# Kernel tuning notes

Measured on AMD Instinct MI355X. Metric: run time of the kernel, lower is better.

Reference implementation:

```python
import jax, jax.numpy as jnp
import numpy as np

THRESHOLD = 0.99


def setup_inputs() -> dict:
    key = jax.random.key(0)
    k1, k2, k3 = jax.random.split(key, 3)
    B, T, D, L = 8, 2048, 1024, 4
    x = jax.random.normal(k1, (B, T, D), dtype=jnp.float32)
    # per-step sub-layer weights (Linear(D, D)), scaled like typical init
    layer_w = jax.random.normal(k2, (L, D, D), dtype=jnp.float32) * (1.0 / np.sqrt(D))
    layer_b = jnp.zeros((L, D), dtype=jnp.float32)
    halt_w = jax.random.normal(k3, (D, 1), dtype=jnp.float32) * (1.0 / np.sqrt(D))
    halt_b = jnp.zeros((1,), dtype=jnp.float32)
    return {"x": x, "layer_w": layer_w, "layer_b": layer_b,
            "halt_w": halt_w, "halt_b": halt_b}


def reference(x, layer_w, layer_b, halt_w, halt_b):
    # Adaptive Computation Time forward.
    # x: (B,T,D); layer_w: (L,D,D); halt_w: (D,1)
    n_steps = layer_w.shape[0]
    B, T, D = x.shape
    dtype = x.dtype
    output = jnp.zeros((B, T, D), dtype=dtype)
    cumulative_halt = jnp.zeros((B, T, 1), dtype=dtype)
    remainder = jnp.ones((B, T, 1), dtype=dtype)
    ponder_steps = jnp.zeros((B, T, 1), dtype=dtype)
    h = x
    for step_idx in range(n_steps):  # small fixed layer count
        # sub-layer: Linear + GELU, (B,T,D) -> (B,T,D)
        h = jax.nn.gelu(jnp.einsum('btd,de->bte', h, layer_w[step_idx]) + layer_b[step_idx])
        # halting unit: Linear(D,1) + sigmoid -> (B,T,1)
        p = jax.nn.sigmoid(h @ halt_w + halt_b)
        if step_idx == n_steps - 1:
            weight = remainder
            contrib = remainder  # all tokens forced to halt
        else:
            halt_mask = (cumulative_halt + p) >= THRESHOLD
            weight = jnp.where(halt_mask, remainder, p)
            contrib = weight
        output = output + weight * h
        ponder_steps = ponder_steps + weight
        cumulative_halt = cumulative_halt + contrib
        remainder = jnp.clip(1.0 - cumulative_halt, 0.0)
    ponder_cost = ponder_steps.mean()
    return output, ponder_cost
```

## Files before the change

### kernel.cpp

```cpp
#include <hip/hip_runtime.h>

typedef __attribute__((ext_vector_type(8))) short short8;
typedef __attribute__((ext_vector_type(4))) float f32x4;
typedef __attribute__((ext_vector_type(4))) unsigned short u16x4;
typedef unsigned short u16;

#define D_DIM 1024
#define NKT 32

__device__ __forceinline__ u16 f2bf(float f) {
  unsigned u = __builtin_bit_cast(unsigned, f);
  u += 0x7fffu + ((u >> 16) & 1u);
  return (u16)(u >> 16);
}
__device__ __forceinline__ float bf2f(u16 b) {
  return __builtin_bit_cast(float, ((unsigned)b) << 16);
}
__device__ __forceinline__ float gelu_f(float x) {
  float i = 0.7978845608028654f * (x + 0.044715f * x * x * x);
  float ex = __builtin_amdgcn_exp2f(i * 2.885390081777927f);
  float th = 1.0f - 2.0f * __builtin_amdgcn_rcpf(ex + 1.0f);
  return 0.5f * x * (1.0f + th);
}
__device__ __forceinline__ f32x4 mfma16(short8 a, short8 b, f32x4 c) {
  return __builtin_amdgcn_mfma_f32_16x16x32_bf16(a, b, c, 0, 0, 0);
}
__device__ __forceinline__ void glds16(const u16* g, const u16* l) {
  __builtin_amdgcn_global_load_lds(
      (const __attribute__((address_space(1))) void*)g,
      (__attribute__((address_space(3))) void*)l, 16, 0, 0);
}

__global__ __launch_bounds__(256) void prep_kernel(
    const float* __restrict__ W, u16* __restrict__ Wth,
    const float* __restrict__ x, u16* __restrict__ xh, int* __restrict__ counts,
    int M) {
  __shared__ float tile[64][65];
  const int bid = blockIdx.x;
  const int t = threadIdx.x;
  if (bid < 1024) {
    const int k0 = (bid & 15) * 64, n0 = ((bid >> 4) & 15) * 64;
    const size_t lbase = (size_t)(bid >> 8) * D_DIM * D_DIM;
#pragma unroll
    for (int j = 0; j < 16; ++j) {
      int idx = t + 256 * j;
      int r = idx >> 6, c = idx & 63;
      tile[r][c] = W[lbase + (size_t)(k0 + r) * D_DIM + (n0 + c)];
    }
    __syncthreads();
#pragma unroll
    for (int j = 0; j < 16; ++j) {
      int idx = t + 256 * j;
      int r = idx >> 6, c = idx & 63;
      Wth[lbase + (size_t)(n0 + r) * D_DIM + (k0 + c)] = f2bf(tile[c][r]);
    }
  } else {
    if (bid == 1024 && t == 0) {
      counts[0] = M;
      counts[1] = M;
    }
    size_t i = ((size_t)(bid - 1024) * 256 + t) * 4;
    const float4 v = *(const float4*)(x + i);
    const float fv[4] = {v.x, v.y, v.z, v.w};
    u16x4 h4;
#pragma unroll
    for (int c = 0; c < 4; ++c) h4[c] = f2bf(fv[c]);
    *(u16x4*)(xh + i) = h4;
  }
}

__global__ __launch_bounds__(256, 4) void gemm_act_kernel(
    const u16* __restrict__ Ahp, const u16* __restrict__ Bhp,
    const float* __restrict__ bias, const float* __restrict__ halt_w,
    u16* __restrict__ Hh, float* __restrict__ zpart,
    const int* __restrict__ srcmap, const int* __restrict__ npadp, int M) {
  extern __shared__ u16 lds[];
  const int bid = blockIdx.x;
  const int mt = (bid & 7) + 8 * (bid >> 6);
  const int bm0 = mt * 128;
  if (bm0 >= *npadp) return;
  const int bn0 = ((bid >> 3) & 7) * 128;
  const int t = threadIdx.x;
  const int lane = t & 63, wid = t >> 6;
  const int wr = wid >> 1, wc = wid & 1;
  const int g = lane >> 4, r16 = lane & 15;

  const int lrow = lane >> 2;
  const int lchunk = (lane & 3) ^ ((lane >> 3) & 3);
  const int u0 = 2 * wid;
  int ar0 = bm0 + 16 * u0 + lrow, ar1 = ar0 + 16;
  if (srcmap) {
    ar0 = srcmap[ar0];
    ar1 = srcmap[ar1];
  }
  const int br0 = bn0 + 16 * u0 + lrow, br1 = br0 + 16;
  const u16* aSh0 = Ahp + (size_t)ar0 * D_DIM + lchunk * 8;
  const u16* aSh1 = Ahp + (size_t)ar1 * D_DIM + lchunk * 8;
  const u16* bSh0 = Bhp + (size_t)br0 * D_DIM + lchunk * 8;
  const u16* bSh1 = Bhp + (size_t)br1 * D_DIM + lchunk * 8;
  const int dst0 = u0 * 512 + lane * 8, dst1 = dst0 + 512;

  const int fsw = ((g ^ (r16 >> 1)) & 3) * 8;
  int a_rd[4], b_rd[4];
#pragma unroll
  for (int i = 0; i < 4; ++i) {
    a_rd[i] = (wr * 64 + i * 16 + r16) * 32 + fsw;
    b_rd[i] = 4096 + (wc * 64 + i * 16 + r16) * 32 + fsw;
  }

  f32x4 acc[4][4];
#pragma unroll
  for (int i = 0; i < 4; ++i)
#pragma unroll
    for (int j = 0; j < 4; ++j) acc[i][j] = (f32x4)0.0f;

  auto stage = [&](int kt) {
    const int k0 = kt << 5;
    u16* db = lds + (kt & 1) * 8192;
    glds16(aSh0 + k0, db + dst0);
    glds16(aSh1 + k0, db + dst1);
    glds16(bSh0 + k0, db + 4096 + dst0);
    glds16(bSh1 + k0, db + 4096 + dst1);
  };
  stage(0);

#pragma unroll 1
  for (int kt = 0; kt < NKT; ++kt) {
    asm volatile("s_waitcnt vmcnt(0)" ::: "memory");
    __builtin_amdgcn_s_barrier();
    asm volatile("" ::: "memory");
    const u16* Lb = lds + (kt & 1) * 8192;
    if (kt + 1 < NKT) stage(kt + 1);
    short8 ah[4], bh[4];
#pragma unroll
    for (int i = 0; i < 4; ++i) {
      ah[i] = *(const short8*)(Lb + a_rd[i]);
      bh[i] = *(const short8*)(Lb + b_rd[i]);
    }
    __builtin_amdgcn_s_setprio(1);
#pragma unroll
    for (int i = 0; i < 4; ++i)
#pragma unroll
      for (int n = 0; n < 4; ++n) acc[i][n] = mfma16(ah[i], bh[n], acc[i][n]);
    __builtin_amdgcn_s_setprio(0);
  }

  __syncthreads();

  float bv[4], hwv[4];
#pragma unroll
  for (int ni = 0; ni < 4; ++ni) {
    int col = bn0 + wc * 64 + ni * 16 + r16;
    bv[ni] = bias[col];
    hwv[ni] = halt_w[col];
  }
  float zp[4][4];
#pragma unroll
  for (int mi = 0; mi < 4; ++mi)
#pragma unroll
    for (int j = 0; j < 4; ++j) {
      float zz = 0.0f;
#pragma unroll
      for (int ni = 0; ni < 4; ++ni) {
        float v = gelu_f(acc[mi][ni][j] + bv[ni]);
        acc[mi][ni][j] = v;
        zz += v * hwv[ni];
      }
      zp[mi][j] = zz;
    }
#pragma unroll
  for (int off = 1; off < 16; off <<= 1)
#pragma unroll
    for (int mi = 0; mi < 4; ++mi)
#pragma unroll
      for (int j = 0; j < 4; ++j) zp[mi][j] += __shfl_xor(zp[mi][j], off);
  float* zf = (float*)lds;
  if (r16 == 0) {
#pragma unroll
    for (int mi = 0; mi < 4; ++mi)
#pragma unroll
      for (int j = 0; j < 4; ++j)
        zf[wc * 128 + wr * 64 + mi * 16 + g * 4 + j] = zp[mi][j];
  }
  __syncthreads();
  if (t < 128) zpart[(size_t)(bn0 >> 7) * M + bm0 + t] = zf[t] + zf[128 + t];
  __syncthreads();

  u16* hp = lds;
#pragma unroll
  for (int mi = 0; mi < 4; ++mi)
#pragma unroll
    for (int ni = 0; ni < 4; ++ni)
#pragma unroll
      for (int j = 0; j < 4; ++j)
        hp[(wr * 64 + mi * 16 + g * 4 + j) * 128 + wc * 64 + ni * 16 + r16] =
            f2bf(acc[mi][ni][j]);
  __syncthreads();
#pragma unroll
  for (int p = 0; p < 8; ++p) {
    int idx = p * 256 + t;
    int r = idx >> 4, c = idx & 15;
    *(short8*)(Hh + (size_t)(bm0 + r) * D_DIM + bn0 + c * 8) =
        *(const short8*)&hp[r * 128 + c * 8];
  }
}

__global__ __launch_bounds__(256) void act_weights_kernel(
    const float* __restrict__ zpart, const float* __restrict__ halt_b,
    float* __restrict__ cum, float* __restrict__ rem, float* __restrict__ pond,
    float* __restrict__ wout, float* __restrict__ wfull,
    int* __restrict__ slotmap, int* __restrict__ last_step,
    const int* __restrict__ idx, const int* __restrict__ np, int step,
    int last, int M) {
  int slot = blockIdx.x * 256 + threadIdx.x;
  if (slot >= *np) return;
  int tok = idx ? idx[slot] : slot;
  float z = halt_b[0];
#pragma unroll
  for (int nb = 0; nb < 8; ++nb) z += zpart[(size_t)nb * M + slot];
  float p = 1.0f / (1.0f + expf(-z));
  float c, r, q;
  if (step == 0) {
    c = 0.0f; r = 1.0f; q = 0.0f;
  } else {
    c = cum[tok]; r = rem[tok]; q = pond[tok];
  }
  float weight = last ? r : (((c + p) >= 0.99f) ? r : p);
  q += weight;
  c += weight;
  r = fmaxf(1.0f - c, 0.0f);
  cum[tok] = c;
  rem[tok] = r;
  pond[tok] = q;
  wout[slot] = weight;
  wfull[(size_t)step * M + tok] = weight;
  slotmap[(size_t)step * M + tok] = slot;
  last_step[tok] = step;
}

__global__ __launch_bounds__(1024) void compact_kernel(
    const float* __restrict__ rem, const int* __restrict__ idx_cur,
    const int* __restrict__ ncur_p, int* __restrict__ idx_next,
    int* __restrict__ src_next, int* __restrict__ cnt_next) {
  __shared__ int sc[1024];
  const int t = threadIdx.x;
  const int n = *ncur_p;
  const int base = t * 16;
  int lc = 0;
#pragma unroll
  for (int i = 0; i < 16; ++i) {
    int j = base + i;
    if (j < n) {
      int tok = idx_cur ? idx_cur[j] : j;
      if (rem[tok] > 0.0f) ++lc;
    }
  }
  sc[t] = lc;
  __syncthreads();
  for (int d = 1; d < 1024; d <<= 1) {
    int v = (t >= d) ? sc[t - d] : 0;
    __syncthreads();
    sc[t] += v;
    __syncthreads();
  }
  int pos = sc[t] - lc;
  const int total = sc[1023];
#pragma unroll
  for (int i = 0; i < 16; ++i) {
    int j = base + i;
    if (j < n) {
      int tok = idx_cur ? idx_cur[j] : j;
      if (rem[tok] > 0.0f) {
        idx_next[pos] = tok;
        src_next[pos] = j;
        ++pos;
      }
    }
  }
  if (t == 0) {
    int pad = (total + 127) & ~127;
    cnt_next[0] = total;
    cnt_next[1] = pad;
    for (int j = total; j < pad; ++j) {
      idx_next[j] = -1;
      src_next[j] = 0;
    }
  }
}

__global__ __launch_bounds__(256) void act_out_kernel(
    const u16* __restrict__ h, const float* __restrict__ w,
    const int* __restrict__ idx, const int* __restrict__ np, int accum,
    float* __restrict__ out) {
  size_t gid = (size_t)blockIdx.x * 256 + threadIdx.x;
  int slot = (int)(gid >> 7);
  if (slot >= *np) return;
  int off = ((int)gid & 127) * 8;
  int tok = idx ? idx[slot] : slot;
  size_t hb = (size_t)slot * D_DIM + off;
  size_t ob = (size_t)tok * D_DIM + off;
  float ws = w[slot];
  short8 hi = *(const short8*)(h + hb);
  float o[8];
  if (accum) {
    float4 a = *(const float4*)(out + ob);
    float4 b = *(const float4*)(out + ob + 4);
    o[0] = a.x; o[1] = a.y; o[2] = a.z; o[3] = a.w;
    o[4] = b.x; o[5] = b.y; o[6] = b.z; o[7] = b.w;
  } else {
#pragma unroll
    for (int j = 0; j < 8; ++j) o[j] = 0.0f;
  }
#pragma unroll
  for (int j = 0; j < 8; ++j) o[j] += ws * bf2f((u16)hi[j]);
  *(float4*)(out + ob) = make_float4(o[0], o[1], o[2], o[3]);
  *(float4*)(out + ob + 4) = make_float4(o[4], o[5], o[6], o[7]);
}

__global__ __launch_bounds__(256) void act_out_final_kernel(
    const u16* __restrict__ h1, const u16* __restrict__ h2,
    const u16* __restrict__ h3, const u16* __restrict__ h4,
    const float* __restrict__ wfull, const int* __restrict__ slotmap,
    const int* __restrict__ last_step, float* __restrict__ out, int M) {
  size_t gid = (size_t)blockIdx.x * 256 + threadIdx.x;
  int tok = (int)(gid >> 7);
  int off = ((int)gid & 127) * 8;
  const int ls = last_step[tok];
  float o[8];
#pragma unroll
  for (int j = 0; j < 8; ++j) o[j] = 0.0f;
  for (int s = 0; s <= ls; ++s) {
    int slot = slotmap[(size_t)s * M + tok];
    float w = wfull[(size_t)s * M + tok];
    const u16* b = (s == 0) ? h1 : (s == 1) ? h2 : (s == 2) ? h3 : h4;
    short8 hv = *(const short8*)(b + (size_t)slot * D_DIM + off);
#pragma unroll
    for (int j = 0; j < 8; ++j) o[j] += w * bf2f((u16)hv[j]);
  }
  size_t ob = (size_t)tok * D_DIM + off;
  *(float4*)(out + ob) = make_float4(o[0], o[1], o[2], o[3]);
  *(float4*)(out + ob + 4) = make_float4(o[4], o[5], o[6], o[7]);
}

__global__ __launch_bounds__(256) void ponder_reduce_kernel(
    const float* __restrict__ pond, float* __restrict__ o, int n) {
  __shared__ float sh[256];
  float a = 0.0f;
  for (int i = threadIdx.x; i < n; i += 256) a += pond[i];
  sh[threadIdx.x] = a;
  __syncthreads();
  for (int s = 128; s; s >>= 1) {
    if ((int)threadIdx.x < s) sh[threadIdx.x] += sh[threadIdx.x + s];
    __syncthreads();
  }
  if (threadIdx.x == 0) o[0] = sh[0] / (float)n;
}

extern "C" void kernel_launch(void* const* d_in, const int* in_sizes, int n_in,
                              void* d_out, int out_size, void* d_ws,
                              size_t ws_size, hipStream_t stream) {
  const float* x = (const float*)d_in[0];
  const float* layer_w = (const float*)d_in[1];
  const float* layer_b = (const float*)d_in[2];
  const float* halt_w = (const float*)d_in[3];
  const float* halt_b = (const float*)d_in[4];
  float* out = (float*)d_out;

  const int D = D_DIM;
  const int M = in_sizes[0] / D;
  const int L = in_sizes[1] / (D * D);
  const size_t MD = (size_t)M * D, DD = (size_t)D * D;

  char* ws = (char*)d_ws;
  size_t off = 0;
  auto alloc = [&](size_t bytes) {
    void* p = ws + off;
    off += (bytes + 255) & ~(size_t)255;
    return p;
  };
  u16* Wth = (u16*)alloc((size_t)L * DD * sizeof(u16));
  float* zpart = (float*)alloc(8 * (size_t)M * 4);
  float* wbuf = (float*)alloc((size_t)M * 4);
  float* wfull = (float*)alloc((size_t)L * M * 4);
  int* slotmap = (int*)alloc((size_t)L * M * 4);
  int* last_step = (int*)alloc((size_t)M * 4);
  float* cum = (float*)alloc((size_t)M * 4);
  float* rem = (float*)alloc((size_t)M * 4);
  float* pond = (float*)alloc((size_t)M * 4);
  int* counts = (int*)alloc(16 * sizeof(int));
  int* idxA = (int*)alloc((size_t)M * 4);
  int* idxB = (int*)alloc((size_t)M * 4);
  int* srcb = (int*)alloc((size_t)M * 4);

  u16* xpair = (u16*)alloc(2 * MD * sizeof(u16));
  const bool deferred = (off + 2 * MD * sizeof(u16) + 4096) <= ws_size;
  u16 *arch = nullptr, *P1 = nullptr;
  if (deferred) {
    arch = (u16*)alloc(2 * MD * sizeof(u16));
  } else {
    P1 = (u16*)alloc(MD * sizeof(u16));
  }
  u16* A[5] = {nullptr, arch, arch ? arch + MD : nullptr, xpair, xpair + MD};

  hipFuncSetAttribute((const void*)gemm_act_kernel,
                      hipFuncAttributeMaxDynamicSharedMemorySize, 32768);

  prep_kernel<<<(unsigned)(1024 + MD / 1024), 256, 0, stream>>>(
      layer_w, Wth, x, xpair, counts, M);

  for (int s = 0; s < L; ++s) {
    const int* idxs = (s == 0) ? nullptr : ((s & 1) ? idxB : idxA);
    const u16* Ahp;
    u16* Hh;
    if (deferred) {
      Ahp = (s == 0) ? xpair : A[s];
      Hh = A[s + 1];
    } else {
      Ahp = (s & 1) ? P1 : xpair;
      Hh = (s & 1) ? xpair : P1;
    }
    gemm_act_kernel<<<dim3((M / 128) * (D / 128)), 256, 32768, stream>>>(
        Ahp, Wth + (size_t)s * DD, layer_b + (size_t)s * D, halt_w, Hh, zpart,
        (s == 0) ? nullptr : srcb, counts + 2 * s + 1, M);
    act_weights_kernel<<<M / 256, 256, 0, stream>>>(
        zpart, halt_b, cum, rem, pond, wbuf, wfull, slotmap, last_step, idxs,
        counts + 2 * s, s, (s == L - 1) ? 1 : 0, M);
    if (!deferred)
      act_out_kernel<<<(unsigned)(MD / 2048), 256, 0, stream>>>(
          Hh, wbuf, idxs, counts + 2 * s, (s > 0) ? 1 : 0, out);
    if (s + 1 < L) {
      int* idxn = ((s + 1) & 1) ? idxB : idxA;
      compact_kernel<<<1, 1024, 0, stream>>>(rem, idxs, counts + 2 * s, idxn,
                                             srcb, counts + 2 * (s + 1));
    }
  }
  if (deferred)
    act_out_final_kernel<<<(unsigned)(MD / 2048), 256, 0, stream>>>(
        A[1], A[2], A[3], A[4], wfull, slotmap, last_step, out, M);
  ponder_reduce_kernel<<<1, 256, 0, stream>>>(pond, out + MD, M);
}
```

Before: 304.8 us.

## Widen GEMM block tile to 128x256 to raise per-block operand reuse

Each GEMM block now computes a 128x256 output tile instead of 128x128. Every warp holds 4x8 accumulator fragments, and the staging loop loads six 16-row chunks per warp into a larger 48KB double-buffered LDS. The intent is to halve redundant A-tile reloads and the grid size, which should cut global/LDS traffic per FLOP. The costs are higher register pressure (launch bounds lowered to 2 blocks per CU), fewer blocks to fill the CUs, and a two-pass epilogue. The halting partial sums drop from 8 to 4 column partitions.

```diff
diff --git a/kernel.cpp b/kernel.cpp
--- a/kernel.cpp
+++ b/kernel.cpp
@@ -69,58 +69,61 @@
   }
 }
 
-__global__ __launch_bounds__(256, 4) void gemm_act_kernel(
+__global__ __launch_bounds__(256, 2) void gemm_act_kernel(
     const u16* __restrict__ Ahp, const u16* __restrict__ Bhp,
     const float* __restrict__ bias, const float* __restrict__ halt_w,
     u16* __restrict__ Hh, float* __restrict__ zpart,
     const int* __restrict__ srcmap, const int* __restrict__ npadp, int M) {
   extern __shared__ u16 lds[];
   const int bid = blockIdx.x;
-  const int mt = (bid & 7) + 8 * (bid >> 6);
+  const int mt = (bid & 7) + 8 * (bid >> 5);
   const int bm0 = mt * 128;
   if (bm0 >= *npadp) return;
-  const int bn0 = ((bid >> 3) & 7) * 128;
+  const int bn0 = ((bid >> 3) & 3) * 256;
   const int t = threadIdx.x;
   const int lane = t & 63, wid = t >> 6;
   const int wr = wid >> 1, wc = wid & 1;
   const int g = lane >> 4, r16 = lane & 15;
 
   const int lrow = lane >> 2;
-  const int lchunk = (lane & 3) ^ ((lane >> 3) & 3);
-  const int u0 = 2 * wid;
-  int ar0 = bm0 + 16 * u0 + lrow, ar1 = ar0 + 16;
-  if (srcmap) {
-    ar0 = srcmap[ar0];
-    ar1 = srcmap[ar1];
-  }
-  const int br0 = bn0 + 16 * u0 + lrow, br1 = br0 + 16;
-  const u16* aSh0 = Ahp + (size_t)ar0 * D_DIM + lchunk * 8;
-  const u16* aSh1 = Ahp + (size_t)ar1 * D_DIM + lchunk * 8;
-  const u16* bSh0 = Bhp + (size_t)br0 * D_DIM + lchunk * 8;
-  const u16* bSh1 = Bhp + (size_t)br1 * D_DIM + lchunk * 8;
-  const int dst0 = u0 * 512 + lane * 8, dst1 = dst0 + 512;
+  const int lchunk = (lane & 3) ^ ((lrow >> 1) & 3);
+  const u16* sb[6];
+  int sd[6];
+#pragma unroll
+  for (int j = 0; j < 6; ++j) {
+    const int u = wid * 6 + j;
+    if (u < 8) {
+      int r = bm0 + 16 * u + lrow;
+      if (srcmap) r = srcmap[r];
+      sb[j] = Ahp + (size_t)r * D_DIM + lchunk * 8;
+      sd[j] = u * 512 + lane * 8;
+    } else {
+      const int v = u - 8;
+      sb[j] = Bhp + (size_t)(bn0 + 16 * v + lrow) * D_DIM + lchunk * 8;
+      sd[j] = 4096 + v * 512 + lane * 8;
+    }
+  }
 
   const int fsw = ((g ^ (r16 >> 1)) & 3) * 8;
-  int a_rd[4], b_rd[4];
+  int a_rd[4], b_rd0[4], b_rd1[4];
 #pragma unroll
   for (int i = 0; i < 4; ++i) {
     a_rd[i] = (wr * 64 + i * 16 + r16) * 32 + fsw;
-    b_rd[i] = 4096 + (wc * 64 + i * 16 + r16) * 32 + fsw;
-  }
-
-  f32x4 acc[4][4];
+    b_rd0[i] = 4096 + (wc * 128 + i * 16 + r16) * 32 + fsw;
+    b_rd1[i] = 4096 + (wc * 128 + 64 + i * 16 + r16) * 32 + fsw;
+  }
+
+  f32x4 acc[4][8];
 #pragma unroll
   for (int i = 0; i < 4; ++i)
 #pragma unroll
-    for (int j = 0; j < 4; ++j) acc[i][j] = (f32x4)0.0f;
+    for (int j = 0; j < 8; ++j) acc[i][j] = (f32x4)0.0f;
 
   auto stage = [&](int kt) {
     const int k0 = kt << 5;
-    u16* db = lds + (kt & 1) * 8192;
-    glds16(aSh0 + k0, db + dst0);
-    glds16(aSh1 + k0, db + dst1);
-    glds16(bSh0 + k0, db + 4096 + dst0);
-    glds16(bSh1 + k0, db + 4096 + dst1);
+    u16* db = lds + (kt & 1) * 12288;
+#pragma unroll
+    for (int j = 0; j < 6; ++j) glds16(sb[j] + k0, db + sd[j]);
   };
   stage(0);
 
@@ -129,13 +132,13 @@
     asm volatile("s_waitcnt vmcnt(0)" ::: "memory");
     __builtin_amdgcn_s_barrier();
     asm volatile("" ::: "memory");
-    const u16* Lb = lds + (kt & 1) * 8192;
+    const u16* Lb = lds + (kt & 1) * 12288;
     if (kt + 1 < NKT) stage(kt + 1);
     short8 ah[4], bh[4];
 #pragma unroll
     for (int i = 0; i < 4; ++i) {
       ah[i] = *(const short8*)(Lb + a_rd[i]);
-      bh[i] = *(const short8*)(Lb + b_rd[i]);
+      bh[i] = *(const short8*)(Lb + b_rd0[i]);
     }
     __builtin_amdgcn_s_setprio(1);
 #pragma unroll
@@ -143,14 +146,23 @@
 #pragma unroll
       for (int n = 0; n < 4; ++n) acc[i][n] = mfma16(ah[i], bh[n], acc[i][n]);
     __builtin_amdgcn_s_setprio(0);
+#pragma unroll
+    for (int i = 0; i < 4; ++i) bh[i] = *(const short8*)(Lb + b_rd1[i]);
+    __builtin_amdgcn_s_setprio(1);
+#pragma unroll
+    for (int i = 0; i < 4; ++i)
+#pragma unroll
+      for (int n = 0; n < 4; ++n)
+        acc[i][4 + n] = mfma16(ah[i], bh[n], acc[i][4 + n]);
+    __builtin_amdgcn_s_setprio(0);
   }
 
   __syncthreads();
 
-  float bv[4], hwv[4];
-#pragma unroll
-  for (int ni = 0; ni < 4; ++ni) {
-    int col = bn0 + wc * 64 + ni * 16 + r16;
+  float bv[8], hwv[8];
+#pragma unroll
+  for (int ni = 0; ni < 8; ++ni) {
+    int col = bn0 + wc * 128 + (ni >> 2) * 64 + (ni & 3) * 16 + r16;
     bv[ni] = bias[col];
     hwv[ni] = halt_w[col];
   }
@@ -161,7 +173,7 @@
     for (int j = 0; j < 4; ++j) {
       float zz = 0.0f;
 #pragma unroll
-      for (int ni = 0; ni < 4; ++ni) {
+      for (int ni = 0; ni < 8; ++ni) {
         float v = gelu_f(acc[mi][ni][j] + bv[ni]);
         acc[mi][ni][j] = v;
         zz += v * hwv[ni];
@@ -183,25 +195,30 @@
         zf[wc * 128 + wr * 64 + mi * 16 + g * 4 + j] = zp[mi][j];
   }
   __syncthreads();
-  if (t < 128) zpart[(size_t)(bn0 >> 7) * M + bm0 + t] = zf[t] + zf[128 + t];
-  __syncthreads();
+  if (t < 128) zpart[(size_t)(bn0 >> 8) * M + bm0 + t] = zf[t] + zf[128 + t];
 
   u16* hp = lds;
-#pragma unroll
-  for (int mi = 0; mi < 4; ++mi)
-#pragma unroll
-    for (int ni = 0; ni < 4; ++ni)
-#pragma unroll
-      for (int j = 0; j < 4; ++j)
-        hp[(wr * 64 + mi * 16 + g * 4 + j) * 128 + wc * 64 + ni * 16 + r16] =
-            f2bf(acc[mi][ni][j]);
-  __syncthreads();
-#pragma unroll
-  for (int p = 0; p < 8; ++p) {
-    int idx = p * 256 + t;
-    int r = idx >> 4, c = idx & 15;
-    *(short8*)(Hh + (size_t)(bm0 + r) * D_DIM + bn0 + c * 8) =
-        *(const short8*)&hp[r * 128 + c * 8];
+#pragma unroll 1
+  for (int H = 0; H < 2; ++H) {
+    __syncthreads();
+    if (wc == H) {
+#pragma unroll
+      for (int mi = 0; mi < 4; ++mi)
+#pragma unroll
+        for (int ni = 0; ni < 8; ++ni)
+#pragma unroll
+          for (int j = 0; j < 4; ++j)
+            hp[(wr * 64 + mi * 16 + g * 4 + j) * 128 + (ni >> 2) * 64 +
+               (ni & 3) * 16 + r16] = f2bf(acc[mi][ni][j]);
+    }
+    __syncthreads();
+#pragma unroll
+    for (int p = 0; p < 8; ++p) {
+      int idx = p * 256 + t;
+      int r = idx >> 4, c = idx & 15;
+      *(short8*)(Hh + (size_t)(bm0 + r) * D_DIM + bn0 + H * 128 + c * 8) =
+          *(const short8*)&hp[r * 128 + c * 8];
+    }
   }
 }
 
@@ -217,7 +234,7 @@
   int tok = idx ? idx[slot] : slot;
   float z = halt_b[0];
 #pragma unroll
-  for (int nb = 0; nb < 8; ++nb) z += zpart[(size_t)nb * M + slot];
+  for (int nb = 0; nb < 4; ++nb) z += zpart[(size_t)nb * M + slot];
   float p = 1.0f / (1.0f + expf(-z));
   float c, r, q;
   if (step == 0) {
@@ -403,7 +420,7 @@
   u16* A[5] = {nullptr, arch, arch ? arch + MD : nullptr, xpair, xpair + MD};
 
   hipFuncSetAttribute((const void*)gemm_act_kernel,
-                      hipFuncAttributeMaxDynamicSharedMemorySize, 32768);
+                      hipFuncAttributeMaxDynamicSharedMemorySize, 49152);
 
   prep_kernel<<<(unsigned)(1024 + MD / 1024), 256, 0, stream>>>(
       layer_w, Wth, x, xpair, counts, M);
@@ -419,7 +436,7 @@
       Ahp = (s & 1) ? P1 : xpair;
       Hh = (s & 1) ? xpair : P1;
     }
-    gemm_act_kernel<<<dim3((M / 128) * (D / 128)), 256, 32768, stream>>>(
+    gemm_act_kernel<<<dim3((M / 128) * (D / 256)), 256, 49152, stream>>>(
         Ahp, Wth + (size_t)s * DD, layer_b + (size_t)s * D, halt_w, Hh, zpart,
         (s == 0) ? nullptr : srcb, counts + 2 * s + 1, M);
     act_weights_kernel<<<M / 256, 256, 0, stream>>>(
```

Measured after the change: 311.9 us. 2.3% more time.
